# Kernel optimization log

Hardware: AMD Instinct MI355X
Metric: run time of the kernel (lower is better)

## Reference

```python
import jax, jax.numpy as jnp
import numpy as np

B, P, DE, DD, DA = 256, 196, 2048, 512, 512

def setup_inputs() -> dict:
    key = jax.random.key(0)
    ks = jax.random.split(key, 8)
    s_enc = 1.0 / np.sqrt(DE)
    s_dec = 1.0 / np.sqrt(DD)
    s_att = 1.0 / np.sqrt(DA)
    return {
        "encoder_out": jax.random.normal(ks[0], (B, P, DE), dtype=jnp.float32),
        "decoder_hidden": jax.random.normal(ks[1], (B, DD), dtype=jnp.float32),
        "W_enc": jax.random.uniform(ks[2], (DE, DA), jnp.float32, -s_enc, s_enc),
        "b_enc": jax.random.uniform(ks[3], (DA,), jnp.float32, -s_enc, s_enc),
        "W_dec": jax.random.uniform(ks[4], (DD, DA), jnp.float32, -s_dec, s_dec),
        "b_dec": jax.random.uniform(ks[5], (DA,), jnp.float32, -s_dec, s_dec),
        "W_full": jax.random.uniform(ks[6], (DA, 1), jnp.float32, -s_att, s_att),
        "b_full": jax.random.uniform(ks[7], (1,), jnp.float32, -s_att, s_att),
    }

def reference(encoder_out, decoder_hidden, W_enc, b_enc, W_dec, b_dec, W_full, b_full):
    # att1: [B,P,DA]; att2: [B,DA]
    att1 = jnp.einsum('bpe,ea->bpa', encoder_out, W_enc) + b_enc
    att2 = decoder_hidden @ W_dec + b_dec
    # broadcast add + relu + project to scalar score per position
    att = jnp.einsum('bpa,a->bp', jax.nn.relu(att1 + att2[:, None, :]), W_full[:, 0]) + b_full[0]
    alpha = jax.nn.softmax(att, axis=1)  # [B,P]
    context_vector = jnp.einsum('bpe,bp->be', encoder_out, alpha)  # [B,DE]
    return (context_vector, alpha)
```

## Files before the change

### kernel.cpp

```cpp
#include <hip/hip_runtime.h>
#include <hip/hip_bf16.h>
#include <cstddef>

#define B_   256
#define P_   196
#define DE_  2048
#define DD_  512
#define DA_  512
#define M_   (B_*P_)

#define BM   64
#define KT   32
#define NKT  (DE_/KT)

typedef __attribute__((ext_vector_type(4))) float f32x4;
typedef __attribute__((ext_vector_type(8))) short s16x8;

static __device__ __forceinline__ short f2bf(float x) {
    __hip_bfloat16 h = __float2bfloat16(x);
    return *reinterpret_cast<short*>(&h);
}

#define GLOAD_LDS16(g, l) __builtin_amdgcn_global_load_lds( \
    (const __attribute__((address_space(1))) void*)(g),     \
    (__attribute__((address_space(3))) void*)(l), 16, 0, 0)

__global__ __launch_bounds__(256) void pack_wenc(
        const float* __restrict__ W, __hip_bfloat16* __restrict__ out) {
    __shared__ float lds[KT][DA_];
    const int kt = blockIdx.x;
    const int t  = threadIdx.x;
#pragma unroll
    for (int i = 0; i < 64; ++i) {
        int e = i * 256 + t;
        int k = e >> 9, n = e & 511;
        lds[k][n] = W[(size_t)(kt * KT + k) * DA_ + n];
    }
    __syncthreads();
    short* o = reinterpret_cast<short*>(out) + (size_t)kt * (32 * 64 * 8);
#pragma unroll
    for (int i = 0; i < 8; ++i) {
        int idx  = i * 256 + t;
        int gf   = idx >> 6;
        int lane = idx & 63;
        int g = lane >> 4, c = lane & 15;
        s16x8 w;
#pragma unroll
        for (int j = 0; j < 8; ++j)
            w[j] = f2bf(lds[g * 8 + j][gf * 16 + c]);
        *reinterpret_cast<s16x8*>(o + (size_t)idx * 8) = w;
    }
}

__global__ __launch_bounds__(512) void att2_kernel(
        const float* __restrict__ dh, const float* __restrict__ W_dec,
        const float* __restrict__ b_dec, const float* __restrict__ b_enc,
        float* __restrict__ att2p) {
    __shared__ float s_dh[DD_];
    const int b = blockIdx.x;
    const int a = threadIdx.x;
    s_dh[a] = dh[(size_t)b * DD_ + a];
    __syncthreads();
    float acc = 0.f;
#pragma unroll 8
    for (int k = 0; k < DD_; ++k)
        acc += s_dh[k] * W_dec[(size_t)k * DA_ + a];
    att2p[(size_t)b * DA_ + a] = acc + b_dec[a] + b_enc[a];
}

__global__ __launch_bounds__(256, 3) void gemm_att(
        const float* __restrict__ enc, const __hip_bfloat16* __restrict__ Bp,
        const float* __restrict__ att2p, const float* __restrict__ Wfull,
        float* __restrict__ att0, float* __restrict__ att1) {
    __shared__ float a_lds[4][BM * KT];
    __shared__ float red[BM][4];

    const int tid  = threadIdx.x;
    const int wave = tid >> 6;
    const int lane = tid & 63;
    const int g    = lane >> 4;
    const int c    = lane & 15;

    const int p   = blockIdx.x;
    const int mt_ = (p >> 4) * 8 + (p & 7);
    const int nh  = (p >> 3) & 1;
    const int block_row = mt_ * BM;

    const int arow  = tid >> 3;
    const int aslot = (tid & 7) ^ (arow & 7);
    const float* a_src = enc + (size_t)(block_row + arow) * DE_ + aslot * 4;

    const int ax  = c & 7;
    const int ao0 = ((2 * g)     ^ ax) * 4;
    const int ao1 = ((2 * g + 1) ^ ax) * 4;

    const s16x8* bp = reinterpret_cast<const s16x8*>(Bp)
                    + ((size_t)(nh * 16 + wave * 4)) * 64 + lane;

    f32x4 acc[4][4] = {};
    s16x8 bfX[4], bfY[4];

#define ISSUE_A(T) do {                                                  \
        const int tt_ = (T) > 63 ? 63 : (T);                             \
        float* d_ = a_lds[(T) & 3];                                      \
        GLOAD_LDS16(a_src + tt_ * KT,                 &d_[tid * 4]);     \
        GLOAD_LDS16(a_src + (size_t)32 * DE_ + tt_ * KT, &d_[(256 + tid) * 4]); \
    } while (0)

#define LOAD_B(dst, T) do {                                              \
        const int tt_ = (T) > 63 ? 63 : (T);                             \
        _Pragma("unroll")                                                \
        for (int n_ = 0; n_ < 4; ++n_)                                   \
            dst[n_] = bp[((size_t)tt_ * 32 + n_) * 64];                  \
    } while (0)

#define COMPUTE(T, bfr) do {                                             \
        const float* ab_ = a_lds[(T) & 3];                               \
        s16x8 af[4];                                                     \
        _Pragma("unroll")                                                \
        for (int mt2 = 0; mt2 < 4; ++mt2) {                              \
            const float* base_ = ab_ + (mt2 * 16 + c) * KT;              \
            f32x4 v0_ = *reinterpret_cast<const f32x4*>(base_ + ao0);    \
            f32x4 v1_ = *reinterpret_cast<const f32x4*>(base_ + ao1);    \
            s16x8 w_;                                                    \
            w_[0]=f2bf(v0_.x); w_[1]=f2bf(v0_.y); w_[2]=f2bf(v0_.z); w_[3]=f2bf(v0_.w); \
            w_[4]=f2bf(v1_.x); w_[5]=f2bf(v1_.y); w_[6]=f2bf(v1_.z); w_[7]=f2bf(v1_.w); \
            af[mt2] = w_;                                                \
        }                                                                \
        _Pragma("unroll")                                                \
        for (int nt2 = 0; nt2 < 4; ++nt2)                                \
            _Pragma("unroll")                                            \
            for (int mt2 = 0; mt2 < 4; ++mt2)                            \
                acc[mt2][nt2] = __builtin_amdgcn_mfma_f32_16x16x32_bf16( \
                                    af[mt2], bfr[nt2], acc[mt2][nt2], 0, 0, 0); \
    } while (0)

#define WAIT6_BAR() do {                                                 \
        asm volatile("s_waitcnt vmcnt(6)" ::: "memory");                 \
        __builtin_amdgcn_s_barrier();                                    \
    } while (0)

    LOAD_B(bfX, 0);
    ISSUE_A(0);
    ISSUE_A(1);
    LOAD_B(bfY, 1);
    WAIT6_BAR();

#pragma clang loop unroll(disable)
    for (int t = 0; t < NKT; t += 2) {
        ISSUE_A(t + 2);
        COMPUTE(t, bfX);
        LOAD_B(bfX, t + 2);
        WAIT6_BAR();
        ISSUE_A(t + 3);
        COMPUTE(t + 1, bfY);
        LOAD_B(bfY, t + 3);
        WAIT6_BAR();
    }

    const int b0    = block_row / P_;
    const int b1    = min(b0 + 1, B_ - 1);
    const int split = (b0 + 1) * P_;
    const int ncol0 = nh * 256 + wave * 64;
    float wf[4], a20[4], a21[4];
#pragma unroll
    for (int nt = 0; nt < 4; ++nt) {
        const int n = ncol0 + nt * 16 + c;
        wf[nt]  = Wfull[n];
        a20[nt] = att2p[(size_t)b0 * DA_ + n];
        a21[nt] = att2p[(size_t)b1 * DA_ + n];
    }
#pragma unroll
    for (int mt = 0; mt < 4; ++mt) {
#pragma unroll
        for (int q = 0; q < 4; ++q) {
            const int row_local = mt * 16 + g * 4 + q;
            const int R = block_row + row_local;
            const bool hiB = (R >= split);
            float s = 0.f;
#pragma unroll
            for (int nt = 0; nt < 4; ++nt) {
                float a2 = hiB ? a21[nt] : a20[nt];
                float v  = acc[mt][nt][q] + a2;
                v = fmaxf(v, 0.f);
                s += v * wf[nt];
            }
#pragma unroll
            for (int off = 1; off < 16; off <<= 1)
                s += __shfl_xor(s, off, 64);
            if (c == 0) red[row_local][wave] = s;
        }
    }
    __syncthreads();
    if (tid < BM) {
        float t = red[tid][0] + red[tid][1] + red[tid][2] + red[tid][3];
        float* dst = nh ? att1 : att0;
        dst[block_row + tid] = t;
    }
#undef ISSUE_A
#undef LOAD_B
#undef COMPUTE
#undef WAIT6_BAR
}

__global__ __launch_bounds__(256) void softmax_kernel(
        const float* __restrict__ att0, const float* __restrict__ att1,
        float* __restrict__ alpha) {
    const int b = blockIdx.x;
    const int t = threadIdx.x;
    __shared__ float sred[4];
    float v = -1e30f;
    if (t < P_) v = att0[(size_t)b * P_ + t] + att1[(size_t)b * P_ + t];
    float m = v;
#pragma unroll
    for (int off = 1; off < 64; off <<= 1) m = fmaxf(m, __shfl_xor(m, off, 64));
    if ((t & 63) == 0) sred[t >> 6] = m;
    __syncthreads();
    const float mall = fmaxf(fmaxf(sred[0], sred[1]), fmaxf(sred[2], sred[3]));
    __syncthreads();
    float e = (t < P_) ? expf(v - mall) : 0.f;
    float s = e;
#pragma unroll
    for (int off = 1; off < 64; off <<= 1) s += __shfl_xor(s, off, 64);
    if ((t & 63) == 0) sred[t >> 6] = s;
    __syncthreads();
    const float stot = sred[0] + sred[1] + sred[2] + sred[3];
    if (t < P_) alpha[(size_t)b * P_ + t] = e / stot;
}

__global__ __launch_bounds__(256) void context_kernel(
        const float* __restrict__ enc, const float* __restrict__ alpha,
        float* __restrict__ ctx) {
    const int b = blockIdx.x;
    const int e = blockIdx.y * 1024 + threadIdx.x * 4;
    __shared__ float s_alpha[P_];
    if (threadIdx.x < P_) s_alpha[threadIdx.x] = alpha[(size_t)b * P_ + threadIdx.x];
    __syncthreads();
    f32x4 acc = {0.f, 0.f, 0.f, 0.f};
    const float* base = enc + (size_t)b * P_ * DE_ + e;
#pragma unroll 4
    for (int p = 0; p < P_; ++p) {
        f32x4 v = *reinterpret_cast<const f32x4*>(base + (size_t)p * DE_);
        acc += s_alpha[p] * v;
    }
    *reinterpret_cast<f32x4*>(ctx + (size_t)b * DE_ + e) = acc;
}

extern "C" void kernel_launch(void* const* d_in, const int* in_sizes, int n_in,
                              void* d_out, int out_size, void* d_ws, size_t ws_size,
                              hipStream_t stream) {
    const float* enc    = (const float*)d_in[0];
    const float* dh     = (const float*)d_in[1];
    const float* W_enc  = (const float*)d_in[2];
    const float* b_enc  = (const float*)d_in[3];
    const float* W_dec  = (const float*)d_in[4];
    const float* b_dec  = (const float*)d_in[5];
    const float* W_full = (const float*)d_in[6];

    float* out       = (float*)d_out;
    float* ctx_out   = out;
    float* alpha_out = out + (size_t)B_ * DE_;

    char* ws = (char*)d_ws;
    __hip_bfloat16* Bp = (__hip_bfloat16*)ws;
    float* att2p = (float*)(ws + 2u * 1024 * 1024);
    float* att0  = (float*)(ws + 2u * 1024 * 1024 + 512u * 1024);
    float* att1  = att0 + M_;

    pack_wenc     <<<NKT,            256, 0, stream>>>(W_enc, Bp);
    att2_kernel   <<<B_,             512, 0, stream>>>(dh, W_dec, b_dec, b_enc, att2p);
    gemm_att      <<<2 * (M_ / BM),  256, 0, stream>>>(enc, Bp, att2p, W_full, att0, att1);
    softmax_kernel<<<B_,             256, 0, stream>>>(att0, att1, alpha_out);
    context_kernel<<<dim3(B_, 2),    256, 0, stream>>>(enc, alpha_out, ctx_out);
}
```

Baseline: 312.0 us.

## Use single-wave GEMM blocks loading A directly into registers, eight column groups

The attention GEMM moves from 256-thread blocks that stage the encoder tile in LDS with barriers to 64-thread single-wave blocks. Each block loads its A fragments straight from global memory into registers and covers one of eight 64-column groups. Partial scores per column group go to an 8-way buffer that the softmax kernel sums, and the MFMA section is wrapped in raised wave priority. This removes LDS traffic and block barriers, but each encoder row tile is now read by eight separate blocks instead of shared across waves, raising global and L2 traffic.

```diff
diff --git a/kernel.cpp b/kernel.cpp
--- a/kernel.cpp
+++ b/kernel.cpp
@@ -9,7 +9,6 @@
 #define DA_  512
 #define M_   (B_*P_)
 
-#define BM   64
 #define KT   32
 #define NKT  (DE_/KT)
 
@@ -20,10 +19,6 @@
     __hip_bfloat16 h = __float2bfloat16(x);
     return *reinterpret_cast<short*>(&h);
 }
-
-#define GLOAD_LDS16(g, l) __builtin_amdgcn_global_load_lds( \
-    (const __attribute__((address_space(1))) void*)(g),     \
-    (__attribute__((address_space(3))) void*)(l), 16, 0, 0)
 
 __global__ __launch_bounds__(256) void pack_wenc(
         const float* __restrict__ W, __hip_bfloat16* __restrict__ out) {
@@ -68,43 +63,34 @@
     att2p[(size_t)b * DA_ + a] = acc + b_dec[a] + b_enc[a];
 }
 
-__global__ __launch_bounds__(256, 3) void gemm_att(
+__global__ __launch_bounds__(64, 2) void gemm_att(
         const float* __restrict__ enc, const __hip_bfloat16* __restrict__ Bp,
         const float* __restrict__ att2p, const float* __restrict__ Wfull,
-        float* __restrict__ att0, float* __restrict__ att1) {
-    __shared__ float a_lds[4][BM * KT];
-    __shared__ float red[BM][4];
-
-    const int tid  = threadIdx.x;
-    const int wave = tid >> 6;
-    const int lane = tid & 63;
+        float* __restrict__ att_part) {
+    const int lane = threadIdx.x;
     const int g    = lane >> 4;
     const int c    = lane & 15;
 
-    const int p   = blockIdx.x;
-    const int mt_ = (p >> 4) * 8 + (p & 7);
-    const int nh  = (p >> 3) & 1;
-    const int block_row = mt_ * BM;
-
-    const int arow  = tid >> 3;
-    const int aslot = (tid & 7) ^ (arow & 7);
-    const float* a_src = enc + (size_t)(block_row + arow) * DE_ + aslot * 4;
-
-    const int ax  = c & 7;
-    const int ao0 = ((2 * g)     ^ ax) * 4;
-    const int ao1 = ((2 * g + 1) ^ ax) * 4;
-
-    const s16x8* bp = reinterpret_cast<const s16x8*>(Bp)
-                    + ((size_t)(nh * 16 + wave * 4)) * 64 + lane;
+    const int bid = blockIdx.x;
+    const int mt_ = (bid >> 6) * 8 + (bid & 7);
+    const int cg  = (bid >> 3) & 7;
+    const int block_row = mt_ * 64;
+
+    const float* aptr = enc + (size_t)(block_row + c) * DE_ + g * 8;
+    const s16x8* bp = reinterpret_cast<const s16x8*>(Bp) + (size_t)(cg * 4) * 64 + lane;
 
     f32x4 acc[4][4] = {};
+    f32x4 paX[4][2], paY[4][2];
     s16x8 bfX[4], bfY[4];
 
-#define ISSUE_A(T) do {                                                  \
+#define LOAD_A(dst, T) do {                                              \
         const int tt_ = (T) > 63 ? 63 : (T);                             \
-        float* d_ = a_lds[(T) & 3];                                      \
-        GLOAD_LDS16(a_src + tt_ * KT,                 &d_[tid * 4]);     \
-        GLOAD_LDS16(a_src + (size_t)32 * DE_ + tt_ * KT, &d_[(256 + tid) * 4]); \
+        _Pragma("unroll")                                                \
+        for (int m_ = 0; m_ < 4; ++m_) {                                 \
+            const float* p_ = aptr + (size_t)m_ * (16 * DE_) + tt_ * KT; \
+            dst[m_][0] = *reinterpret_cast<const f32x4*>(p_);            \
+            dst[m_][1] = *reinterpret_cast<const f32x4*>(p_ + 4);        \
+        }                                                                \
     } while (0)
 
 #define LOAD_B(dst, T) do {                                              \
@@ -114,103 +100,92 @@
             dst[n_] = bp[((size_t)tt_ * 32 + n_) * 64];                  \
     } while (0)
 
-#define COMPUTE(T, bfr) do {                                             \
-        const float* ab_ = a_lds[(T) & 3];                               \
+#define STEP(pa, bfr) do {                                               \
         s16x8 af[4];                                                     \
         _Pragma("unroll")                                                \
-        for (int mt2 = 0; mt2 < 4; ++mt2) {                              \
-            const float* base_ = ab_ + (mt2 * 16 + c) * KT;              \
-            f32x4 v0_ = *reinterpret_cast<const f32x4*>(base_ + ao0);    \
-            f32x4 v1_ = *reinterpret_cast<const f32x4*>(base_ + ao1);    \
+        for (int m_ = 0; m_ < 4; ++m_) {                                 \
             s16x8 w_;                                                    \
-            w_[0]=f2bf(v0_.x); w_[1]=f2bf(v0_.y); w_[2]=f2bf(v0_.z); w_[3]=f2bf(v0_.w); \
-            w_[4]=f2bf(v1_.x); w_[5]=f2bf(v1_.y); w_[6]=f2bf(v1_.z); w_[7]=f2bf(v1_.w); \
-            af[mt2] = w_;                                                \
+            w_[0]=f2bf(pa[m_][0].x); w_[1]=f2bf(pa[m_][0].y);            \
+            w_[2]=f2bf(pa[m_][0].z); w_[3]=f2bf(pa[m_][0].w);            \
+            w_[4]=f2bf(pa[m_][1].x); w_[5]=f2bf(pa[m_][1].y);            \
+            w_[6]=f2bf(pa[m_][1].z); w_[7]=f2bf(pa[m_][1].w);            \
+            af[m_] = w_;                                                 \
         }                                                                \
-        _Pragma("unroll")                                                \
-        for (int nt2 = 0; nt2 < 4; ++nt2)                                \
+        __builtin_amdgcn_s_setprio(1);                                   \
+        _Pragma("unroll")                                                \
+        for (int n_ = 0; n_ < 4; ++n_)                                   \
             _Pragma("unroll")                                            \
-            for (int mt2 = 0; mt2 < 4; ++mt2)                            \
-                acc[mt2][nt2] = __builtin_amdgcn_mfma_f32_16x16x32_bf16( \
-                                    af[mt2], bfr[nt2], acc[mt2][nt2], 0, 0, 0); \
+            for (int m_ = 0; m_ < 4; ++m_)                               \
+                acc[m_][n_] = __builtin_amdgcn_mfma_f32_16x16x32_bf16(   \
+                                  af[m_], bfr[n_], acc[m_][n_], 0, 0, 0);\
+        __builtin_amdgcn_s_setprio(0);                                   \
     } while (0)
 
-#define WAIT6_BAR() do {                                                 \
-        asm volatile("s_waitcnt vmcnt(6)" ::: "memory");                 \
-        __builtin_amdgcn_s_barrier();                                    \
-    } while (0)
-
+    LOAD_A(paX, 0);
     LOAD_B(bfX, 0);
-    ISSUE_A(0);
-    ISSUE_A(1);
+    LOAD_A(paY, 1);
     LOAD_B(bfY, 1);
-    WAIT6_BAR();
 
 #pragma clang loop unroll(disable)
     for (int t = 0; t < NKT; t += 2) {
-        ISSUE_A(t + 2);
-        COMPUTE(t, bfX);
+        STEP(paX, bfX);
+        LOAD_A(paX, t + 2);
         LOAD_B(bfX, t + 2);
-        WAIT6_BAR();
-        ISSUE_A(t + 3);
-        COMPUTE(t + 1, bfY);
+        STEP(paY, bfY);
+        LOAD_A(paY, t + 3);
         LOAD_B(bfY, t + 3);
-        WAIT6_BAR();
     }
 
     const int b0    = block_row / P_;
     const int b1    = min(b0 + 1, B_ - 1);
     const int split = (b0 + 1) * P_;
-    const int ncol0 = nh * 256 + wave * 64;
     float wf[4], a20[4], a21[4];
 #pragma unroll
-    for (int nt = 0; nt < 4; ++nt) {
-        const int n = ncol0 + nt * 16 + c;
-        wf[nt]  = Wfull[n];
-        a20[nt] = att2p[(size_t)b0 * DA_ + n];
-        a21[nt] = att2p[(size_t)b1 * DA_ + n];
-    }
+    for (int n = 0; n < 4; ++n) {
+        const int col = cg * 64 + n * 16 + c;
+        wf[n]  = Wfull[col];
+        a20[n] = att2p[(size_t)b0 * DA_ + col];
+        a21[n] = att2p[(size_t)b1 * DA_ + col];
+    }
+    float* dst = att_part + (size_t)cg * M_ + block_row;
 #pragma unroll
     for (int mt = 0; mt < 4; ++mt) {
 #pragma unroll
         for (int q = 0; q < 4; ++q) {
             const int row_local = mt * 16 + g * 4 + q;
-            const int R = block_row + row_local;
-            const bool hiB = (R >= split);
+            const bool hiB = (block_row + row_local >= split);
             float s = 0.f;
 #pragma unroll
-            for (int nt = 0; nt < 4; ++nt) {
-                float a2 = hiB ? a21[nt] : a20[nt];
-                float v  = acc[mt][nt][q] + a2;
+            for (int n = 0; n < 4; ++n) {
+                float a2 = hiB ? a21[n] : a20[n];
+                float v  = acc[mt][n][q] + a2;
                 v = fmaxf(v, 0.f);
-                s += v * wf[nt];
+                s += v * wf[n];
             }
 #pragma unroll
             for (int off = 1; off < 16; off <<= 1)
                 s += __shfl_xor(s, off, 64);
-            if (c == 0) red[row_local][wave] = s;
+            if (c == 0) dst[row_local] = s;
         }
     }
-    __syncthreads();
-    if (tid < BM) {
-        float t = red[tid][0] + red[tid][1] + red[tid][2] + red[tid][3];
-        float* dst = nh ? att1 : att0;
-        dst[block_row + tid] = t;
-    }
-#undef ISSUE_A
+#undef LOAD_A
 #undef LOAD_B
-#undef COMPUTE
-#undef WAIT6_BAR
+#undef STEP
 }
 
 __global__ __launch_bounds__(256) void softmax_kernel(
-        const float* __restrict__ att0, const float* __restrict__ att1,
-        float* __restrict__ alpha) {
+        const float* __restrict__ att_part, float* __restrict__ alpha) {
     const int b = blockIdx.x;
     const int t = threadIdx.x;
     __shared__ float sred[4];
     float v = -1e30f;
-    if (t < P_) v = att0[(size_t)b * P_ + t] + att1[(size_t)b * P_ + t];
+    if (t < P_) {
+        const size_t R = (size_t)b * P_ + t;
+        v = 0.f;
+#pragma unroll
+        for (int cgi = 0; cgi < 8; ++cgi)
+            v += att_part[(size_t)cgi * M_ + R];
+    }
     float m = v;
 #pragma unroll
     for (int off = 1; off < 64; off <<= 1) m = fmaxf(m, __shfl_xor(m, off, 64));
@@ -262,14 +237,13 @@
     float* alpha_out = out + (size_t)B_ * DE_;
 
     char* ws = (char*)d_ws;
-    __hip_bfloat16* Bp = (__hip_bfloat16*)ws;
-    float* att2p = (float*)(ws + 2u * 1024 * 1024);
-    float* att0  = (float*)(ws + 2u * 1024 * 1024 + 512u * 1024);
-    float* att1  = att0 + M_;
+    __hip_bfloat16* Bp  = (__hip_bfloat16*)ws;
+    float* att2p    = (float*)(ws + 2u * 1024 * 1024);
+    float* att_part = (float*)(ws + 2u * 1024 * 1024 + 512u * 1024);
 
     pack_wenc     <<<NKT,            256, 0, stream>>>(W_enc, Bp);
     att2_kernel   <<<B_,             512, 0, stream>>>(dh, W_dec, b_dec, b_enc, att2p);
-    gemm_att      <<<2 * (M_ / BM),  256, 0, stream>>>(enc, Bp, att2p, W_full, att0, att1);
-    softmax_kernel<<<B_,             256, 0, stream>>>(att0, att1, alpha_out);
+    gemm_att      <<<(M_ / 64) * 8,  64,  0, stream>>>(enc, Bp, att2p, W_full, att_part);
+    softmax_kernel<<<B_,             256, 0, stream>>>(att_part, alpha_out);
     context_kernel<<<dim3(B_, 2),    256, 0, stream>>>(enc, alpha_out, ctx_out);
 }
```

Result: slower. 558.3 us (+78.9%).
